# Kernel tuning notes

Hardware: AMD Instinct MI355X
Metric: run time of the kernel (lower is better)

Reference implementation:

```python
import jax, jax.numpy as jnp
import numpy as np

LS, LT, B = 48, 48, 64
VS, VT = 32000, 32000
E = 512      # src/tgt embed dim
HE = 512     # encoder hidden (BiLSTM -> context dim 2*HE)
HD = 512     # decoder hidden
PAD = 0


def setup_inputs() -> dict:
    key = jax.random.key(0)
    ks = iter(jax.random.split(key, 24))
    w = lambda *shape: jax.random.normal(next(ks), shape, dtype=jnp.float32) * 0.05
    inp = {}
    inp["xs"] = jax.random.randint(next(ks), (LS, B), 0, VS)
    inp["ts"] = jax.random.randint(next(ks), (LT, B), 0, VT)
    # embeddings (padding row zeroed, as nn.Embedding(padding_idx=0))
    inp["src_emb"] = w(VS, E).at[PAD].set(0.0)
    inp["tgt_emb"] = w(VT, E).at[PAD].set(0.0)
    # forward / backward encoder LSTMCells
    for p in ("encf", "encb"):
        inp[p + "_Wih"] = w(4 * HE, E)
        inp[p + "_Whh"] = w(4 * HE, HE)
        inp[p + "_bih"] = w(4 * HE)
        inp[p + "_bhh"] = w(4 * HE)
    # decoder LSTMCell: input = [tgt_emb ; o] -> E + HD
    inp["dec_Wih"] = w(4 * HD, E + HD)
    inp["dec_Whh"] = w(4 * HD, HD)
    inp["dec_bih"] = w(4 * HD)
    inp["dec_bhh"] = w(4 * HD)
    # MLPAttention: linear [2HE, HD+2HE] (no bias), v [1, 2HE] (no bias)
    inp["attn_W"] = w(2 * HE, HD + 2 * HE)
    inp["attn_v"] = w(1, 2 * HE)
    # decoder.linear: [HD, HD+2HE] with bias
    inp["lin_W"] = w(HD, HD + 2 * HE)
    inp["lin_b"] = w(HD)
    # decoder.linear_out: [VT, HD] with bias
    inp["out_W"] = w(VT, HD)
    inp["out_b"] = w(VT)
    return inp


def _lstm_cell(x, h, c, Wih, Whh, bih, bhh):
    g = x @ Wih.T + h @ Whh.T + (bih + bhh)
    i, f, gg, o = jnp.split(g, 4, axis=-1)  # torch gate order i,f,g,o
    c = jax.nn.sigmoid(f) * c + jax.nn.sigmoid(i) * jnp.tanh(gg)
    h = jax.nn.sigmoid(o) * jnp.tanh(c)
    return h, c


def _lstm_scan(embs, Wih, Whh, bih, bhh, hidden):
    bsz = embs.shape[1]
    init = (jnp.zeros((bsz, hidden), embs.dtype), jnp.zeros((bsz, hidden), embs.dtype))
    def step(carry, x):
        h, c = _lstm_cell(x, carry[0], carry[1], Wih, Whh, bih, bhh)
        return (h, c), h
    _, hs = jax.lax.scan(step, init, embs)
    return hs  # [L, B, hidden]


def reference(xs, ts, src_emb, tgt_emb,
              encf_Wih, encf_Whh, encf_bih, encf_bhh,
              encb_Wih, encb_Whh, encb_bih, encb_bhh,
              dec_Wih, dec_Whh, dec_bih, dec_bhh,
              attn_W, attn_v, lin_W, lin_b, out_W, out_b):
    # ---- BiLSTM encoder ----
    embs = src_emb[xs]                                   # [LS, B, E]
    hs_f = _lstm_scan(embs, encf_Wih, encf_Whh, encf_bih, encf_bhh, HE)
    hs_b = _lstm_scan(embs[::-1], encb_Wih, encb_Whh, encb_bih, encb_bhh, HE)[::-1]
    hs = jnp.concatenate([hs_f, hs_b], axis=2)           # [LS, B, 2HE]
    hs_bt = hs.transpose(1, 0, 2)                        # [B, LS, 2HE]

    # attention linear splits: cat((query, hs)) -> first HD cols act on query
    Wq, Wk = attn_W[:, :HD], attn_W[:, HD:]
    hs_proj = jnp.einsum('blk,hk->blh', hs_bt, Wk)       # precompute key part
    v = attn_v[0]

    ts_in, ts_out = ts[:-1], ts[1:]
    bsz = ts.shape[1]
    init = (jnp.zeros((bsz, HD), jnp.float32),) * 3      # h, m, o

    def dec_step(carry, t):
        h, m, o = carry
        emb = tgt_emb[t]                                 # [B, E]
        h, m = _lstm_cell(jnp.concatenate([emb, o], 1), h, m,
                          dec_Wih, dec_Whh, dec_bih, dec_bhh)
        # MLP attention
        score = jnp.tanh(hs_proj + (h @ Wq.T)[:, None, :]) @ v   # [B, LS]
        ps = jax.nn.softmax(score, axis=-1)
        c = jnp.einsum('bl,blh->bh', ps, hs_bt)          # [B, 2HE]
        o = jnp.tanh(jnp.concatenate([c, h], 1) @ lin_W.T + lin_b)
        logits = h @ out_W.T + out_b                     # [B, VT]
        return (h, m, o), logits

    _, logits = jax.lax.scan(dec_step, init, ts_in)      # [LT-1, B, VT]
    logp = jax.nn.log_softmax(logits, axis=-1)

    # NLLLoss(ignore_index=PAD), mean over non-pad targets
    nll = -jnp.take_along_axis(logp, ts_out[..., None], axis=-1)[..., 0]
    mask = (ts_out != PAD).astype(logp.dtype)
    return jnp.sum(nll * mask) / jnp.sum(mask)
```

## Files before the change

kernel.cpp:

```cpp
#include <hip/hip_runtime.h>
#include <stdint.h>

typedef unsigned short us;
typedef __attribute__((ext_vector_type(8))) short bf16x8;
typedef __attribute__((ext_vector_type(4))) float f32x4;

#define DI __device__ __forceinline__

constexpr int LS = 48, LT = 48, NB = 64, E = 512, H = 512, G = 2048, V = 32000;
constexpr int TD = LT - 1;
constexpr int MENC = LS * NB;
constexpr int MDEC = TD * NB;
constexpr int NCB = V / 64;

DI float bf2f(us u) { union { unsigned int i; float f; } c; c.i = ((unsigned int)u) << 16; return c.f; }
DI us f2bf(float f) { union { float f; unsigned int i; } c; c.f = f; return (us)((c.i + 0x7fffu + ((c.i >> 16) & 1u)) >> 16); }
DI float sigm(float x) { return 1.f / (1.f + __expf(-x)); }
DI float tanh_(float x) { x = fminf(15.f, fmaxf(-15.f, x)); float e = __expf(2.f * x); return (e - 1.f) / (e + 1.f); }

__global__ __launch_bounds__(256) void zero_k(float* p, int n) {
    int i = blockIdx.x * 256 + threadIdx.x;
    if (i < n) p[i] = 0.f;
}

__global__ __launch_bounds__(256) void conv_bf16(const float* __restrict__ src, int lds, int coff,
                                                 us* __restrict__ dst, int rows, int cols) {
    int i = blockIdx.x * 256 + threadIdx.x;
    if (i >= rows * cols) return;
    int r = i / cols, c = i % cols;
    dst[i] = f2bf(src[(size_t)r * lds + coff + c]);
}

__global__ __launch_bounds__(256) void gather_bf16(const int* __restrict__ idx, const float* __restrict__ emb,
                                                   us* __restrict__ dst) {
    int r = blockIdx.x;
    int id = idx[r];
    const float* s = emb + (size_t)id * E;
    us* d = dst + (size_t)r * E;
    for (int c = threadIdx.x; c < E; c += 256) d[c] = f2bf(s[c]);
}

__global__ __launch_bounds__(256) void pack_wcomb(const float* __restrict__ Wih, const float* __restrict__ Whh,
                                                  float* __restrict__ Wc) {
    int i = blockIdx.x * 256 + threadIdx.x;
    int j = i >> 10, c = i & 1023;
    Wc[i] = (c < 512) ? Wih[(size_t)j * 1024 + 512 + c] : Whh[(size_t)j * 512 + (c - 512)];
}

template <int EPI>
__global__ __launch_bounds__(256) void gemm16(const us* __restrict__ A, int lda,
                                              const us* __restrict__ W, int ldw,
                                              const float* __restrict__ b1, const float* __restrict__ b2,
                                              void* __restrict__ outp, int ldc, int K, int Mrows) {
    __shared__ us As[64][40];
    __shared__ us Ws[64][40];
    const int tid = threadIdx.x;
    const int m0 = blockIdx.y << 6, n0 = blockIdx.x << 6;
    const int srow = tid >> 2, sk = (tid & 3) << 3;
    const int l = tid & 63, w = tid >> 6;
    const int la = l & 15, lb = l >> 4;
    f32x4 acc[4] = {};
    const us* Aptr = A + (size_t)(m0 + srow) * lda + sk;
    const us* Wptr = W + (size_t)(n0 + srow) * ldw + sk;
    for (int k0 = 0; k0 < K; k0 += 32) {
        *(uint4*)&As[srow][sk] = *(const uint4*)(Aptr + k0);
        *(uint4*)&Ws[srow][sk] = *(const uint4*)(Wptr + k0);
        __syncthreads();
        bf16x8 af = *(bf16x8*)&As[(w << 4) + la][lb << 3];
#pragma unroll
        for (int c = 0; c < 4; c++) {
            bf16x8 bw = *(bf16x8*)&Ws[(c << 4) + la][lb << 3];
            acc[c] = __builtin_amdgcn_mfma_f32_16x16x32_bf16(af, bw, acc[c], 0, 0, 0);
        }
        __syncthreads();
    }
    if (EPI == 1) {
        us* O = (us*)outp;
#pragma unroll
        for (int c = 0; c < 4; c++) {
            int col = n0 + (c << 4) + la;
            float badd = (b1 ? b1[col] : 0.f) + (b2 ? b2[col] : 0.f);
#pragma unroll
            for (int r = 0; r < 4; r++) {
                int row = m0 + (w << 4) + (lb << 2) + r;
                O[(size_t)row * ldc + col] = f2bf(acc[c][r] + badd);
            }
        }
    } else {
        float* S = (float*)outp;
        float x[4][4];
#pragma unroll
        for (int c = 0; c < 4; c++) {
            int col = n0 + (c << 4) + la;
            float badd = b1[col];
#pragma unroll
            for (int r = 0; r < 4; r++) x[c][r] = acc[c][r] + badd;
        }
#pragma unroll
        for (int r = 0; r < 4; r++) {
            float lm = fmaxf(fmaxf(x[0][r], x[1][r]), fmaxf(x[2][r], x[3][r]));
#pragma unroll
            for (int mk = 1; mk < 16; mk <<= 1) lm = fmaxf(lm, __shfl_xor(lm, mk));
            float ls = __expf(x[0][r] - lm) + __expf(x[1][r] - lm) + __expf(x[2][r] - lm) + __expf(x[3][r] - lm);
#pragma unroll
            for (int mk = 1; mk < 16; mk <<= 1) ls += __shfl_xor(ls, mk);
            if (la == 0) {
                int row = m0 + (w << 4) + (lb << 2) + r;
                size_t o = ((size_t)blockIdx.x * Mrows + row) * 2;
                S[o] = lm;
                S[o + 1] = ls;
            }
        }
    }
}

__global__ __launch_bounds__(256) void enc_step(const us* __restrict__ gxf, const us* __restrict__ gxb,
                                                const float* __restrict__ Whhf, const float* __restrict__ Whhb,
                                                const float* __restrict__ hinf, const float* __restrict__ hinb,
                                                float* __restrict__ houtf, float* __restrict__ houtb,
                                                float* __restrict__ cf, float* __restrict__ cb_,
                                                float* __restrict__ hs, us* __restrict__ hs_bf, int s) {
    const int dir = blockIdx.z;
    const us* gx = dir ? gxb : gxf;
    const float* Whh = dir ? Whhb : Whhf;
    const float* hin = dir ? hinb : hinf;
    float* hout = dir ? houtb : houtf;
    float* cst = dir ? cb_ : cf;
    const int lrow = dir ? (LS - 1 - s) : s;
    __shared__ float hls[16][516];
    const int tid = threadIdx.x;
    const int bl = tid & 15, jl = tid >> 4;
    const int b0 = blockIdx.y * 16;
    const int j = blockIdx.x * 16 + jl;
    for (int idx = tid; idx < 16 * 512; idx += 256) { int r = idx >> 9, c = idx & 511; hls[r][c] = hin[(size_t)(b0 + r) * 512 + c]; }
    __syncthreads();
    const int b = b0 + bl;
    const us* grow = gx + ((size_t)lrow * NB + b) * G;
    float ai = bf2f(grow[j]), af = bf2f(grow[512 + j]), ag = bf2f(grow[1024 + j]), ao = bf2f(grow[1536 + j]);
    const float* wi = Whh + (size_t)j * 512;
    const float* wf = Whh + (size_t)(512 + j) * 512;
    const float* wg = Whh + (size_t)(1024 + j) * 512;
    const float* wo = Whh + (size_t)(1536 + j) * 512;
    for (int k = 0; k < 512; k += 4) {
        float4 h4 = *(float4*)&hls[bl][k];
        float4 a = *(const float4*)&wi[k]; ai += a.x * h4.x + a.y * h4.y + a.z * h4.z + a.w * h4.w;
        float4 f = *(const float4*)&wf[k]; af += f.x * h4.x + f.y * h4.y + f.z * h4.z + f.w * h4.w;
        float4 g = *(const float4*)&wg[k]; ag += g.x * h4.x + g.y * h4.y + g.z * h4.z + g.w * h4.w;
        float4 o = *(const float4*)&wo[k]; ao += o.x * h4.x + o.y * h4.y + o.z * h4.z + o.w * h4.w;
    }
    const int ci = b * 512 + j;
    float cn = sigm(af) * cst[ci] + sigm(ai) * tanh_(ag);
    float hn = sigm(ao) * tanh_(cn);
    cst[ci] = cn;
    hout[ci] = hn;
    size_t hso = ((size_t)lrow * NB + b) * 1024 + dir * 512 + j;
    hs[hso] = hn;
    hs_bf[hso] = f2bf(hn);
}

__global__ __launch_bounds__(256) void dec_cell(const us* __restrict__ gemb, const float* __restrict__ Wcomb,
                                                const float* __restrict__ oin, const float* __restrict__ hin,
                                                float* __restrict__ hout, float* __restrict__ cst,
                                                us* __restrict__ hdec_bf, int t) {
    __shared__ float uls[8][1028];
    const int tid = threadIdx.x;
    const int bl = tid & 7, jl = tid >> 3;
    const int b0 = blockIdx.y * 8;
    const int j = blockIdx.x * 32 + jl;
    for (int idx = tid; idx < 8 * 1024; idx += 256) {
        int r = idx >> 10, c = idx & 1023;
        uls[r][c] = (c < 512) ? oin[(size_t)(b0 + r) * 512 + c] : hin[(size_t)(b0 + r) * 512 + (c - 512)];
    }
    __syncthreads();
    const int b = b0 + bl;
    const us* grow = gemb + ((size_t)t * NB + b) * G;
    float ai = bf2f(grow[j]), af = bf2f(grow[512 + j]), ag = bf2f(grow[1024 + j]), ao = bf2f(grow[1536 + j]);
    const float* wi = Wcomb + (size_t)j * 1024;
    const float* wf = Wcomb + (size_t)(512 + j) * 1024;
    const float* wg = Wcomb + (size_t)(1024 + j) * 1024;
    const float* wo = Wcomb + (size_t)(1536 + j) * 1024;
    for (int k = 0; k < 1024; k += 4) {
        float4 h4 = *(float4*)&uls[bl][k];
        float4 a = *(const float4*)&wi[k]; ai += a.x * h4.x + a.y * h4.y + a.z * h4.z + a.w * h4.w;
        float4 f = *(const float4*)&wf[k]; af += f.x * h4.x + f.y * h4.y + f.z * h4.z + f.w * h4.w;
        float4 g = *(const float4*)&wg[k]; ag += g.x * h4.x + g.y * h4.y + g.z * h4.z + g.w * h4.w;
        float4 o = *(const float4*)&wo[k]; ao += o.x * h4.x + o.y * h4.y + o.z * h4.z + o.w * h4.w;
    }
    const int ci = b * 512 + j;
    float cn = sigm(af) * cst[ci] + sigm(ai) * tanh_(ag);
    float hn = sigm(ao) * tanh_(cn);
    cst[ci] = cn;
    hout[ci] = hn;
    hdec_bf[((size_t)t * NB + b) * 512 + j] = f2bf(hn);
}

template <int ACT>
__global__ __launch_bounds__(256) void small_gemm(const float* __restrict__ U1, int K1,
                                                  const float* __restrict__ U2, int K2,
                                                  const float* __restrict__ W, int ldw,
                                                  const float* __restrict__ bias,
                                                  float* __restrict__ out, int ldo) {
    extern __shared__ float uls[];
    const int K = K1 + K2;
    const int stride = K + 4;
    const int tid = threadIdx.x;
    for (int r = 0; r < 8; r++) {
        int gb = blockIdx.y * 8 + r;
        for (int c = tid; c < K; c += 256) {
            float v = (c < K1) ? U1[(size_t)gb * K1 + c] : U2[(size_t)gb * K2 + (c - K1)];
            uls[r * stride + c] = v;
        }
    }
    __syncthreads();
    const int bl = tid & 7, jl = tid >> 3;
    const int b = blockIdx.y * 8 + bl;
    const int n = blockIdx.x * 32 + jl;
    const float* wr = W + (size_t)n * ldw;
    float acc = 0.f;
    for (int k = 0; k < K; k += 4) {
        float4 u = *(float4*)&uls[bl * stride + k];
        float4 wv = *(const float4*)&wr[k];
        acc += u.x * wv.x + u.y * wv.y + u.z * wv.z + u.w * wv.w;
    }
    if (bias) acc += bias[n];
    if (ACT == 1) acc = tanh_(acc);
    out[(size_t)b * ldo + n] = acc;
}

__global__ __launch_bounds__(256) void dec_attn(const float* __restrict__ qbuf, const us* __restrict__ hsproj,
                                                const float* __restrict__ hs, const float* __restrict__ vat,
                                                float* __restrict__ catt) {
    const int b = blockIdx.x;
    const int tid = threadIdx.x;
    const int w = tid >> 6, l = tid & 63;
    __shared__ float sc[48];
    __shared__ float ps[48];
    float qv[16], vv[16];
#pragma unroll
    for (int i = 0; i < 16; i++) { qv[i] = qbuf[(size_t)b * 1024 + l * 16 + i]; vv[i] = vat[l * 16 + i]; }
    for (int li = w * 12; li < w * 12 + 12; ++li) {
        const us* hp = hsproj + ((size_t)li * NB + b) * 1024 + l * 16;
        float p = 0.f;
#pragma unroll
        for (int i = 0; i < 16; i++) p += vv[i] * tanh_(bf2f(hp[i]) + qv[i]);
#pragma unroll
        for (int m = 1; m < 64; m <<= 1) p += __shfl_xor(p, m);
        if (l == 0) sc[li] = p;
    }
    __syncthreads();
    if (w == 0) {
        float x = (l < 48) ? sc[l] : -1e30f;
        float mx = x;
#pragma unroll
        for (int m = 1; m < 64; m <<= 1) mx = fmaxf(mx, __shfl_xor(mx, m));
        float e = (l < 48) ? __expf(x - mx) : 0.f;
        float s = e;
#pragma unroll
        for (int m = 1; m < 64; m <<= 1) s += __shfl_xor(s, m);
        if (l < 48) ps[l] = e / s;
    }
    __syncthreads();
    float a0 = 0, a1 = 0, a2 = 0, a3 = 0;
    for (int li = 0; li < 48; ++li) {
        float p = ps[li];
        float4 hv = *(const float4*)(hs + ((size_t)li * NB + b) * 1024 + tid * 4);
        a0 += p * hv.x; a1 += p * hv.y; a2 += p * hv.z; a3 += p * hv.w;
    }
    float4 r; r.x = a0; r.y = a1; r.z = a2; r.w = a3;
    *(float4*)(catt + (size_t)b * 1024 + tid * 4) = r;
}

__global__ __launch_bounds__(256) void tgt_kernel(const us* __restrict__ hdec_bf, const us* __restrict__ woutbf,
                                                  const float* __restrict__ out_b, const int* __restrict__ ts,
                                                  float* __restrict__ tgt) {
    int wid = blockIdx.x * 4 + (threadIdx.x >> 6);
    int l = threadIdx.x & 63;
    int t = wid >> 6, b = wid & 63;
    int tg = ts[(t + 1) * NB + b];
    const us* hr = hdec_bf + (size_t)wid * 512 + l * 8;
    const us* wr = woutbf + (size_t)tg * 512 + l * 8;
    float acc = 0.f;
#pragma unroll
    for (int i = 0; i < 8; i++) acc += bf2f(hr[i]) * bf2f(wr[i]);
#pragma unroll
    for (int m = 1; m < 64; m <<= 1) acc += __shfl_xor(acc, m);
    if (l == 0) tgt[wid] = acc + out_b[tg];
}

__global__ __launch_bounds__(256) void stats_reduce(const float* __restrict__ stats, const float* __restrict__ tgt,
                                                    const int* __restrict__ ts, float* __restrict__ sums) {
    int r = blockIdx.x * 256 + threadIdx.x;
    float nll = 0.f, mk = 0.f;
    if (r < MDEC) {
        float M = -1e30f, S = 0.f;
        for (int cb = 0; cb < NCB; ++cb) {
            float m = stats[((size_t)cb * MDEC + r) * 2];
            float s = stats[((size_t)cb * MDEC + r) * 2 + 1];
            if (m > M) { S = S * __expf(M - m) + s; M = m; }
            else { S += s * __expf(m - M); }
        }
        float logZ = M + __logf(S);
        int t = r >> 6, b = r & 63;
        int tg = ts[(t + 1) * NB + b];
        mk = (tg != 0) ? 1.f : 0.f;
        nll = (logZ - tgt[r]) * mk;
    }
#pragma unroll
    for (int m = 1; m < 64; m <<= 1) { nll += __shfl_xor(nll, m); mk += __shfl_xor(mk, m); }
    if ((threadIdx.x & 63) == 0) { atomicAdd(&sums[0], nll); atomicAdd(&sums[1], mk); }
}

__global__ void final_div(const float* __restrict__ sums, float* __restrict__ out) { out[0] = sums[0] / sums[1]; }

extern "C" void kernel_launch(void* const* d_in, const int* in_sizes, int n_in,
                              void* d_out, int out_size, void* d_ws, size_t ws_size,
                              hipStream_t stream) {
    const int* xs = (const int*)d_in[0];
    const int* ts = (const int*)d_in[1];
    const float* src_emb = (const float*)d_in[2];
    const float* tgt_emb = (const float*)d_in[3];
    const float* encf_Wih = (const float*)d_in[4];
    const float* encf_Whh = (const float*)d_in[5];
    const float* encf_bih = (const float*)d_in[6];
    const float* encf_bhh = (const float*)d_in[7];
    const float* encb_Wih = (const float*)d_in[8];
    const float* encb_Whh = (const float*)d_in[9];
    const float* encb_bih = (const float*)d_in[10];
    const float* encb_bhh = (const float*)d_in[11];
    const float* dec_Wih = (const float*)d_in[12];
    const float* dec_Whh = (const float*)d_in[13];
    const float* dec_bih = (const float*)d_in[14];
    const float* dec_bhh = (const float*)d_in[15];
    const float* attn_W = (const float*)d_in[16];
    const float* attn_v = (const float*)d_in[17];
    const float* lin_W = (const float*)d_in[18];
    const float* lin_b = (const float*)d_in[19];
    const float* out_W = (const float*)d_in[20];
    const float* out_b = (const float*)d_in[21];

    char* p = (char*)d_ws;
    auto alloc = [&](size_t bytes) { void* r = (void*)p; p += (bytes + 255) & ~(size_t)255; return r; };

    float* hf0 = (float*)alloc(NB * 512 * 4);
    float* hb0 = (float*)alloc(NB * 512 * 4);
    float* cf = (float*)alloc(NB * 512 * 4);
    float* cb = (float*)alloc(NB * 512 * 4);
    float* hd0 = (float*)alloc(NB * 512 * 4);
    float* cd = (float*)alloc(NB * 512 * 4);
    float* od = (float*)alloc(NB * 512 * 4);
    float* sums = (float*)alloc(2 * 4);
    const int ZN = 7 * NB * 512 + 64;

    float* hf1 = (float*)alloc(NB * 512 * 4);
    float* hb1 = (float*)alloc(NB * 512 * 4);
    float* hd1 = (float*)alloc(NB * 512 * 4);
    float* wcomb = (float*)alloc((size_t)G * 1024 * 4);
    float* hs = (float*)alloc((size_t)MENC * 1024 * 4);
    float* qbuf = (float*)alloc((size_t)NB * 1024 * 4);
    float* catt = (float*)alloc((size_t)NB * 1024 * 4);
    float* stats = (float*)alloc((size_t)NCB * MDEC * 2 * 4);
    float* tgtl = (float*)alloc((size_t)MDEC * 4);

    us* embs_bf = (us*)alloc((size_t)MENC * E * 2);
    us* tembs_bf = (us*)alloc((size_t)MDEC * E * 2);
    us* wfih_bf = (us*)alloc((size_t)G * 512 * 2);
    us* wbih_bf = (us*)alloc((size_t)G * 512 * 2);
    us* wdE_bf = (us*)alloc((size_t)G * 512 * 2);
    us* wk_bf = (us*)alloc((size_t)1024 * 1024 * 2);
    us* wout_bf = (us*)alloc((size_t)V * 512 * 2);
    us* gxf_bf = (us*)alloc((size_t)MENC * G * 2);
    us* gxb_bf = (us*)alloc((size_t)MENC * G * 2);
    us* gemb_bf = (us*)alloc((size_t)MDEC * G * 2);
    us* hs_bf = (us*)alloc((size_t)MENC * 1024 * 2);
    us* hsproj_bf = (us*)alloc((size_t)MENC * 1024 * 2);
    us* hdec_bf = (us*)alloc((size_t)MDEC * 512 * 2);

    zero_k<<<dim3((ZN + 255) / 256), 256, 0, stream>>>(hf0, ZN);

    conv_bf16<<<dim3((G * 512 + 255) / 256), 256, 0, stream>>>(encf_Wih, 512, 0, wfih_bf, G, 512);
    conv_bf16<<<dim3((G * 512 + 255) / 256), 256, 0, stream>>>(encb_Wih, 512, 0, wbih_bf, G, 512);
    conv_bf16<<<dim3((G * 512 + 255) / 256), 256, 0, stream>>>(dec_Wih, 1024, 0, wdE_bf, G, 512);
    conv_bf16<<<dim3((1024 * 1024 + 255) / 256), 256, 0, stream>>>(attn_W, 1536, 512, wk_bf, 1024, 1024);
    conv_bf16<<<dim3((V * 512 + 255) / 256), 256, 0, stream>>>(out_W, 512, 0, wout_bf, V, 512);
    pack_wcomb<<<dim3(G * 1024 / 256), 256, 0, stream>>>(dec_Wih, dec_Whh, wcomb);

    gather_bf16<<<dim3(MENC), 256, 0, stream>>>(xs, src_emb, embs_bf);
    gather_bf16<<<dim3(MDEC), 256, 0, stream>>>(ts, tgt_emb, tembs_bf);

    gemm16<1><<<dim3(G / 64, MENC / 64), 256, 0, stream>>>(embs_bf, 512, wfih_bf, 512, encf_bih, encf_bhh, gxf_bf, G, 512, 0);
    gemm16<1><<<dim3(G / 64, MENC / 64), 256, 0, stream>>>(embs_bf, 512, wbih_bf, 512, encb_bih, encb_bhh, gxb_bf, G, 512, 0);
    gemm16<1><<<dim3(G / 64, MDEC / 64), 256, 0, stream>>>(tembs_bf, 512, wdE_bf, 512, dec_bih, dec_bhh, gemb_bf, G, 512, 0);

    for (int s = 0; s < LS; ++s) {
        const float* hinf = (s & 1) ? hf1 : hf0; float* houtf = (s & 1) ? hf0 : hf1;
        const float* hinb = (s & 1) ? hb1 : hb0; float* houtb = (s & 1) ? hb0 : hb1;
        enc_step<<<dim3(32, 4, 2), 256, 0, stream>>>(gxf_bf, gxb_bf, encf_Whh, encb_Whh,
                                                     hinf, hinb, houtf, houtb, cf, cb, hs, hs_bf, s);
    }

    gemm16<1><<<dim3(1024 / 64, MENC / 64), 256, 0, stream>>>(hs_bf, 1024, wk_bf, 1024, nullptr, nullptr, hsproj_bf, 1024, 1024, 0);

    for (int t = 0; t < TD; ++t) {
        const float* hin = (t & 1) ? hd1 : hd0; float* hout = (t & 1) ? hd0 : hd1;
        dec_cell<<<dim3(16, 8), 256, 0, stream>>>(gemb_bf, wcomb, od, hin, hout, cd, hdec_bf, t);
        if (t < TD - 1) {
            small_gemm<0><<<dim3(32, 8), 256, (512 + 4) * 8 * 4, stream>>>(hout, 512, nullptr, 0, attn_W, 1536, nullptr, qbuf, 1024);
            dec_attn<<<dim3(NB), 256, 0, stream>>>(qbuf, hsproj_bf, hs, attn_v, catt);
            small_gemm<1><<<dim3(16, 8), 256, (1536 + 4) * 8 * 4, stream>>>(catt, 1024, hout, 512, lin_W, 1536, lin_b, od, 512);
        }
    }

    gemm16<2><<<dim3(NCB, MDEC / 64), 256, 0, stream>>>(hdec_bf, 512, wout_bf, 512, out_b, nullptr, stats, 0, 512, MDEC);

    tgt_kernel<<<dim3(MDEC / 4), 256, 0, stream>>>(hdec_bf, wout_bf, out_b, ts, tgtl);
    stats_reduce<<<dim3((MDEC + 255) / 256), 256, 0, stream>>>(stats, tgtl, ts, sums);
    final_div<<<dim3(1), 1, 0, stream>>>(sums, (float*)d_out);
}
```

Before: 7.473 ms.

## Replace per-step encoder/decoder launches with persistent cooperative kernels using grid sync

The encoder loop of 48 launches and the decoder loop of roughly 188 launches become two persistent cooperative kernels. Each kernel keeps its cell state in registers and uses grid-wide syncs between steps and phases. The decoder kernel fuses the LSTM cell, query projection, attention and output linear, splits K across lane pairs, and reads lin_W and the context from bf16 copies, which drops the fp32 hs buffer. This removes launch overhead and intermediate round-trips, at the cost of grid-sync latency and some bf16 precision loss in the attention context and linear layer.

```diff
diff --git a/kernel.cpp b/kernel.cpp
--- a/kernel.cpp
+++ b/kernel.cpp
@@ -1,5 +1,8 @@
 #include <hip/hip_runtime.h>
+#include <hip/hip_cooperative_groups.h>
 #include <stdint.h>
+
+namespace cg = cooperative_groups;
 
 typedef unsigned short us;
 typedef __attribute__((ext_vector_type(8))) short bf16x8;
@@ -7,7 +10,7 @@
 
 #define DI __device__ __forceinline__
 
-constexpr int LS = 48, LT = 48, NB = 64, E = 512, H = 512, G = 2048, V = 32000;
+constexpr int LS = 48, LT = 48, NB = 64, E = 512, G = 2048, V = 32000;
 constexpr int TD = LT - 1;
 constexpr int MENC = LS * NB;
 constexpr int MDEC = TD * NB;
@@ -114,160 +117,191 @@
     }
 }
 
-__global__ __launch_bounds__(256) void enc_step(const us* __restrict__ gxf, const us* __restrict__ gxb,
+__global__ __launch_bounds__(256) void enc_coop(const us* __restrict__ gxf, const us* __restrict__ gxb,
                                                 const float* __restrict__ Whhf, const float* __restrict__ Whhb,
-                                                const float* __restrict__ hinf, const float* __restrict__ hinb,
-                                                float* __restrict__ houtf, float* __restrict__ houtb,
-                                                float* __restrict__ cf, float* __restrict__ cb_,
-                                                float* __restrict__ hs, us* __restrict__ hs_bf, int s) {
-    const int dir = blockIdx.z;
+                                                float* __restrict__ hA, float* __restrict__ hB,
+                                                us* __restrict__ hs_bf) {
+    cg::grid_group gg = cg::this_grid();
+    const int bx = blockIdx.x;
+    const int jt = bx & 31, btile = (bx >> 5) & 3, dir = bx >> 7;
     const us* gx = dir ? gxb : gxf;
     const float* Whh = dir ? Whhb : Whhf;
-    const float* hin = dir ? hinb : hinf;
-    float* hout = dir ? houtb : houtf;
-    float* cst = dir ? cb_ : cf;
-    const int lrow = dir ? (LS - 1 - s) : s;
+    const int tid = threadIdx.x, bl = tid & 15, jl = tid >> 4;
+    const int b0 = btile * 16, b = b0 + bl, j = jt * 16 + jl;
     __shared__ float hls[16][516];
-    const int tid = threadIdx.x;
-    const int bl = tid & 15, jl = tid >> 4;
-    const int b0 = blockIdx.y * 16;
-    const int j = blockIdx.x * 16 + jl;
-    for (int idx = tid; idx < 16 * 512; idx += 256) { int r = idx >> 9, c = idx & 511; hls[r][c] = hin[(size_t)(b0 + r) * 512 + c]; }
-    __syncthreads();
-    const int b = b0 + bl;
-    const us* grow = gx + ((size_t)lrow * NB + b) * G;
-    float ai = bf2f(grow[j]), af = bf2f(grow[512 + j]), ag = bf2f(grow[1024 + j]), ao = bf2f(grow[1536 + j]);
+    float cstate = 0.f;
     const float* wi = Whh + (size_t)j * 512;
     const float* wf = Whh + (size_t)(512 + j) * 512;
     const float* wg = Whh + (size_t)(1024 + j) * 512;
     const float* wo = Whh + (size_t)(1536 + j) * 512;
-    for (int k = 0; k < 512; k += 4) {
-        float4 h4 = *(float4*)&hls[bl][k];
-        float4 a = *(const float4*)&wi[k]; ai += a.x * h4.x + a.y * h4.y + a.z * h4.z + a.w * h4.w;
-        float4 f = *(const float4*)&wf[k]; af += f.x * h4.x + f.y * h4.y + f.z * h4.z + f.w * h4.w;
-        float4 g = *(const float4*)&wg[k]; ag += g.x * h4.x + g.y * h4.y + g.z * h4.z + g.w * h4.w;
-        float4 o = *(const float4*)&wo[k]; ao += o.x * h4.x + o.y * h4.y + o.z * h4.z + o.w * h4.w;
-    }
-    const int ci = b * 512 + j;
-    float cn = sigm(af) * cst[ci] + sigm(ai) * tanh_(ag);
-    float hn = sigm(ao) * tanh_(cn);
-    cst[ci] = cn;
-    hout[ci] = hn;
-    size_t hso = ((size_t)lrow * NB + b) * 1024 + dir * 512 + j;
-    hs[hso] = hn;
-    hs_bf[hso] = f2bf(hn);
-}
-
-__global__ __launch_bounds__(256) void dec_cell(const us* __restrict__ gemb, const float* __restrict__ Wcomb,
-                                                const float* __restrict__ oin, const float* __restrict__ hin,
-                                                float* __restrict__ hout, float* __restrict__ cst,
-                                                us* __restrict__ hdec_bf, int t) {
-    __shared__ float uls[8][1028];
+    const size_t dof = (size_t)dir * NB * 512;
+    for (int s = 0; s < LS; ++s) {
+        const float* hin = ((s & 1) ? hB : hA) + dof;
+        float* hout = ((s & 1) ? hA : hB) + dof;
+        const int lrow = dir ? (LS - 1 - s) : s;
+        for (int idx = tid; idx < 16 * 512; idx += 256) {
+            int r = idx >> 9, c = idx & 511;
+            hls[r][c] = hin[(size_t)(b0 + r) * 512 + c];
+        }
+        __syncthreads();
+        const us* grow = gx + ((size_t)lrow * NB + b) * G;
+        float ai = bf2f(grow[j]), af = bf2f(grow[512 + j]), ag = bf2f(grow[1024 + j]), ao = bf2f(grow[1536 + j]);
+        for (int k = 0; k < 512; k += 4) {
+            float4 h4 = *(float4*)&hls[bl][k];
+            float4 a = *(const float4*)&wi[k]; ai += a.x * h4.x + a.y * h4.y + a.z * h4.z + a.w * h4.w;
+            float4 f = *(const float4*)&wf[k]; af += f.x * h4.x + f.y * h4.y + f.z * h4.z + f.w * h4.w;
+            float4 g = *(const float4*)&wg[k]; ag += g.x * h4.x + g.y * h4.y + g.z * h4.z + g.w * h4.w;
+            float4 o = *(const float4*)&wo[k]; ao += o.x * h4.x + o.y * h4.y + o.z * h4.z + o.w * h4.w;
+        }
+        float cn = sigm(af) * cstate + sigm(ai) * tanh_(ag);
+        float hn = sigm(ao) * tanh_(cn);
+        cstate = cn;
+        hout[(size_t)b * 512 + j] = hn;
+        hs_bf[((size_t)lrow * NB + b) * 1024 + dir * 512 + j] = f2bf(hn);
+        gg.sync();
+    }
+}
+
+__global__ __launch_bounds__(256) void dec_coop(const us* __restrict__ gemb, const float* __restrict__ Wcomb,
+                                                const float* __restrict__ attn_W, const float* __restrict__ attn_v,
+                                                const us* __restrict__ hsproj, const us* __restrict__ hs_bf,
+                                                const us* __restrict__ linw_bf, const float* __restrict__ lin_b,
+                                                float* __restrict__ h0, float* __restrict__ h1,
+                                                float* __restrict__ od, float* __restrict__ qbuf,
+                                                us* __restrict__ hdec_bf) {
+    cg::grid_group gg = cg::this_grid();
     const int tid = threadIdx.x;
-    const int bl = tid & 7, jl = tid >> 3;
-    const int b0 = blockIdx.y * 8;
-    const int j = blockIdx.x * 32 + jl;
-    for (int idx = tid; idx < 8 * 1024; idx += 256) {
-        int r = idx >> 10, c = idx & 1023;
-        uls[r][c] = (c < 512) ? oin[(size_t)(b0 + r) * 512 + c] : hin[(size_t)(b0 + r) * 512 + (c - 512)];
-    }
-    __syncthreads();
-    const int b = b0 + bl;
-    const us* grow = gemb + ((size_t)t * NB + b) * G;
-    float ai = bf2f(grow[j]), af = bf2f(grow[512 + j]), ag = bf2f(grow[1024 + j]), ao = bf2f(grow[1536 + j]);
-    const float* wi = Wcomb + (size_t)j * 1024;
-    const float* wf = Wcomb + (size_t)(512 + j) * 1024;
-    const float* wg = Wcomb + (size_t)(1024 + j) * 1024;
-    const float* wo = Wcomb + (size_t)(1536 + j) * 1024;
-    for (int k = 0; k < 1024; k += 4) {
-        float4 h4 = *(float4*)&uls[bl][k];
-        float4 a = *(const float4*)&wi[k]; ai += a.x * h4.x + a.y * h4.y + a.z * h4.z + a.w * h4.w;
-        float4 f = *(const float4*)&wf[k]; af += f.x * h4.x + f.y * h4.y + f.z * h4.z + f.w * h4.w;
-        float4 g = *(const float4*)&wg[k]; ag += g.x * h4.x + g.y * h4.y + g.z * h4.z + g.w * h4.w;
-        float4 o = *(const float4*)&wo[k]; ao += o.x * h4.x + o.y * h4.y + o.z * h4.z + o.w * h4.w;
-    }
-    const int ci = b * 512 + j;
-    float cn = sigm(af) * cst[ci] + sigm(ai) * tanh_(ag);
-    float hn = sigm(ao) * tanh_(cn);
-    cst[ci] = cn;
-    hout[ci] = hn;
-    hdec_bf[((size_t)t * NB + b) * 512 + j] = f2bf(hn);
-}
-
-template <int ACT>
-__global__ __launch_bounds__(256) void small_gemm(const float* __restrict__ U1, int K1,
-                                                  const float* __restrict__ U2, int K2,
-                                                  const float* __restrict__ W, int ldw,
-                                                  const float* __restrict__ bias,
-                                                  float* __restrict__ out, int ldo) {
-    extern __shared__ float uls[];
-    const int K = K1 + K2;
-    const int stride = K + 4;
-    const int tid = threadIdx.x;
-    for (int r = 0; r < 8; r++) {
-        int gb = blockIdx.y * 8 + r;
-        for (int c = tid; c < K; c += 256) {
-            float v = (c < K1) ? U1[(size_t)gb * K1 + c] : U2[(size_t)gb * K2 + (c - K1)];
-            uls[r * stride + c] = v;
-        }
-    }
-    __syncthreads();
-    const int bl = tid & 7, jl = tid >> 3;
-    const int b = blockIdx.y * 8 + bl;
-    const int n = blockIdx.x * 32 + jl;
-    const float* wr = W + (size_t)n * ldw;
-    float acc = 0.f;
-    for (int k = 0; k < K; k += 4) {
-        float4 u = *(float4*)&uls[bl * stride + k];
-        float4 wv = *(const float4*)&wr[k];
-        acc += u.x * wv.x + u.y * wv.y + u.z * wv.z + u.w * wv.w;
-    }
-    if (bias) acc += bias[n];
-    if (ACT == 1) acc = tanh_(acc);
-    out[(size_t)b * ldo + n] = acc;
-}
-
-__global__ __launch_bounds__(256) void dec_attn(const float* __restrict__ qbuf, const us* __restrict__ hsproj,
-                                                const float* __restrict__ hs, const float* __restrict__ vat,
-                                                float* __restrict__ catt) {
-    const int b = blockIdx.x;
-    const int tid = threadIdx.x;
-    const int w = tid >> 6, l = tid & 63;
-    __shared__ float sc[48];
-    __shared__ float ps[48];
-    float qv[16], vv[16];
-#pragma unroll
-    for (int i = 0; i < 16; i++) { qv[i] = qbuf[(size_t)b * 1024 + l * 16 + i]; vv[i] = vat[l * 16 + i]; }
-    for (int li = w * 12; li < w * 12 + 12; ++li) {
-        const us* hp = hsproj + ((size_t)li * NB + b) * 1024 + l * 16;
-        float p = 0.f;
-#pragma unroll
-        for (int i = 0; i < 16; i++) p += vv[i] * tanh_(bf2f(hp[i]) + qv[i]);
-#pragma unroll
-        for (int m = 1; m < 64; m <<= 1) p += __shfl_xor(p, m);
-        if (l == 0) sc[li] = p;
-    }
-    __syncthreads();
-    if (w == 0) {
-        float x = (l < 48) ? sc[l] : -1e30f;
-        float mx = x;
-#pragma unroll
-        for (int m = 1; m < 64; m <<= 1) mx = fmaxf(mx, __shfl_xor(mx, m));
-        float e = (l < 48) ? __expf(x - mx) : 0.f;
-        float s = e;
-#pragma unroll
-        for (int m = 1; m < 64; m <<= 1) s += __shfl_xor(s, m);
-        if (l < 48) ps[l] = e / s;
-    }
-    __syncthreads();
-    float a0 = 0, a1 = 0, a2 = 0, a3 = 0;
-    for (int li = 0; li < 48; ++li) {
-        float p = ps[li];
-        float4 hv = *(const float4*)(hs + ((size_t)li * NB + b) * 1024 + tid * 4);
-        a0 += p * hv.x; a1 += p * hv.y; a2 += p * hv.z; a3 += p * hv.w;
-    }
-    float4 r; r.x = a0; r.y = a1; r.z = a2; r.w = a3;
-    *(float4*)(catt + (size_t)b * 1024 + tid * 4) = r;
+    const int bx = blockIdx.x;
+    __shared__ float uls[8][1044];
+    __shared__ float u2ls[1544];
+    __shared__ float sls[48], pls[48];
+
+    const int khA = tid & 1, blA = (tid >> 1) & 7, jlA = tid >> 4;
+    const int bgrp = bx >> 5, jt = bx & 31;
+    const int bA = bgrp * 8 + blA, jA = jt * 16 + jlA;
+    const int blB = tid & 7, nlB = tid >> 3;
+    const int bB = bgrp * 8 + blB, nB = jt * 32 + nlB;
+    const int bC = bx >> 2, qtr = bx & 3;
+    const int wC = tid >> 6, lC = tid & 63;
+
+    float cstate = 0.f;
+    const float* wiA = Wcomb + ((size_t)jA) * 1024 + khA * 512;
+    const float* wfA = Wcomb + ((size_t)(512 + jA)) * 1024 + khA * 512;
+    const float* wgA = Wcomb + ((size_t)(1024 + jA)) * 1024 + khA * 512;
+    const float* woA = Wcomb + ((size_t)(1536 + jA)) * 1024 + khA * 512;
+
+    float vv[16];
+#pragma unroll
+    for (int i = 0; i < 16; i++) vv[i] = attn_v[lC * 16 + i];
+
+    for (int t = 0; t < TD; ++t) {
+        const float* hprev = (t & 1) ? h1 : h0;
+        float* hnext = (t & 1) ? h0 : h1;
+        {
+            const int b0 = bgrp * 8;
+            for (int idx = tid; idx < 8 * 1024; idx += 256) {
+                int r = idx >> 10, c = idx & 1023;
+                uls[r][c] = (c < 512) ? od[(size_t)(b0 + r) * 512 + c]
+                                      : hprev[(size_t)(b0 + r) * 512 + (c - 512)];
+            }
+            __syncthreads();
+            float ai = 0.f, af = 0.f, ag = 0.f, ao = 0.f;
+            const float* u = &uls[blA][khA * 512];
+            for (int k = 0; k < 512; k += 4) {
+                float4 h4 = *(float4*)&u[k];
+                float4 a = *(const float4*)&wiA[k]; ai += a.x * h4.x + a.y * h4.y + a.z * h4.z + a.w * h4.w;
+                float4 f = *(const float4*)&wfA[k]; af += f.x * h4.x + f.y * h4.y + f.z * h4.z + f.w * h4.w;
+                float4 g = *(const float4*)&wgA[k]; ag += g.x * h4.x + g.y * h4.y + g.z * h4.z + g.w * h4.w;
+                float4 o = *(const float4*)&woA[k]; ao += o.x * h4.x + o.y * h4.y + o.z * h4.z + o.w * h4.w;
+            }
+            ai += __shfl_xor(ai, 1); af += __shfl_xor(af, 1);
+            ag += __shfl_xor(ag, 1); ao += __shfl_xor(ao, 1);
+            if (khA == 0) {
+                const us* grow = gemb + ((size_t)t * NB + bA) * G;
+                ai += bf2f(grow[jA]); af += bf2f(grow[512 + jA]);
+                ag += bf2f(grow[1024 + jA]); ao += bf2f(grow[1536 + jA]);
+                float cn = sigm(af) * cstate + sigm(ai) * tanh_(ag);
+                float hn = sigm(ao) * tanh_(cn);
+                cstate = cn;
+                hnext[(size_t)bA * 512 + jA] = hn;
+                hdec_bf[((size_t)t * NB + bA) * 512 + jA] = f2bf(hn);
+            }
+        }
+        gg.sync();
+        if (t < TD - 1) {
+            for (int idx = tid; idx < 8 * 512; idx += 256) {
+                int r = idx >> 9, c = idx & 511;
+                uls[r][c] = hnext[(size_t)(bgrp * 8 + r) * 512 + c];
+            }
+            __syncthreads();
+            const float* wq = attn_W + (size_t)nB * 1536;
+            const float* u = &uls[blB][0];
+            float acc = 0.f;
+            for (int k = 0; k < 512; k += 4) {
+                float4 h4 = *(float4*)&u[k];
+                float4 wv = *(const float4*)&wq[k];
+                acc += h4.x * wv.x + h4.y * wv.y + h4.z * wv.z + h4.w * wv.w;
+            }
+            qbuf[(size_t)bB * 1024 + nB] = acc;
+        }
+        gg.sync();
+        if (t < TD - 1) {
+            float qv[16];
+#pragma unroll
+            for (int i = 0; i < 16; i++) qv[i] = qbuf[(size_t)bC * 1024 + lC * 16 + i];
+            for (int c = tid; c < 512; c += 256) u2ls[1024 + c] = hnext[(size_t)bC * 512 + c];
+            for (int li = wC * 12; li < wC * 12 + 12; ++li) {
+                const us* hp = hsproj + ((size_t)li * NB + bC) * 1024 + lC * 16;
+                float p = 0.f;
+#pragma unroll
+                for (int i = 0; i < 16; i++) p += vv[i] * tanh_(bf2f(hp[i]) + qv[i]);
+#pragma unroll
+                for (int m = 1; m < 64; m <<= 1) p += __shfl_xor(p, m);
+                if (lC == 0) sls[li] = p;
+            }
+            __syncthreads();
+            if (wC == 0) {
+                float x = (lC < 48) ? sls[lC] : -1e30f;
+                float mx = x;
+#pragma unroll
+                for (int m = 1; m < 64; m <<= 1) mx = fmaxf(mx, __shfl_xor(mx, m));
+                float e = (lC < 48) ? __expf(x - mx) : 0.f;
+                float s = e;
+#pragma unroll
+                for (int m = 1; m < 64; m <<= 1) s += __shfl_xor(s, m);
+                if (lC < 48) pls[lC] = e / s;
+            }
+            __syncthreads();
+            {
+                int d0 = tid * 4;
+                float a0 = 0, a1 = 0, a2 = 0, a3 = 0;
+                for (int li = 0; li < 48; ++li) {
+                    float pw = pls[li];
+                    const us* hv = hs_bf + ((size_t)li * NB + bC) * 1024 + d0;
+                    a0 += pw * bf2f(hv[0]); a1 += pw * bf2f(hv[1]);
+                    a2 += pw * bf2f(hv[2]); a3 += pw * bf2f(hv[3]);
+                }
+                u2ls[d0] = a0; u2ls[d0 + 1] = a1; u2ls[d0 + 2] = a2; u2ls[d0 + 3] = a3;
+            }
+            __syncthreads();
+            {
+                int d = qtr * 128 + (tid >> 1);
+                int kh2 = tid & 1;
+                const us* wr = linw_bf + (size_t)d * 1536 + kh2 * 768;
+                const float* u2 = &u2ls[kh2 * 768];
+                float acc = 0.f;
+                for (int k = 0; k < 768; k += 8) {
+                    float4 ua = *(const float4*)&u2[k];
+                    float4 ub = *(const float4*)&u2[k + 4];
+                    acc += bf2f(wr[k]) * ua.x + bf2f(wr[k + 1]) * ua.y + bf2f(wr[k + 2]) * ua.z + bf2f(wr[k + 3]) * ua.w;
+                    acc += bf2f(wr[k + 4]) * ub.x + bf2f(wr[k + 5]) * ub.y + bf2f(wr[k + 6]) * ub.z + bf2f(wr[k + 7]) * ub.w;
+                }
+                acc += __shfl_xor(acc, 1);
+                if (kh2 == 0) od[(size_t)bC * 512 + d] = tanh_(acc + lin_b[d]);
+            }
+        }
+        gg.sync();
+    }
 }
 
 __global__ __launch_bounds__(256) void tgt_kernel(const us* __restrict__ hdec_bf, const us* __restrict__ woutbf,
@@ -343,21 +377,16 @@
 
     float* hf0 = (float*)alloc(NB * 512 * 4);
     float* hb0 = (float*)alloc(NB * 512 * 4);
-    float* cf = (float*)alloc(NB * 512 * 4);
-    float* cb = (float*)alloc(NB * 512 * 4);
     float* hd0 = (float*)alloc(NB * 512 * 4);
-    float* cd = (float*)alloc(NB * 512 * 4);
     float* od = (float*)alloc(NB * 512 * 4);
     float* sums = (float*)alloc(2 * 4);
-    const int ZN = 7 * NB * 512 + 64;
+    const int ZN = 4 * NB * 512 + 64;
 
     float* hf1 = (float*)alloc(NB * 512 * 4);
     float* hb1 = (float*)alloc(NB * 512 * 4);
     float* hd1 = (float*)alloc(NB * 512 * 4);
     float* wcomb = (float*)alloc((size_t)G * 1024 * 4);
-    float* hs = (float*)alloc((size_t)MENC * 1024 * 4);
     float* qbuf = (float*)alloc((size_t)NB * 1024 * 4);
-    float* catt = (float*)alloc((size_t)NB * 1024 * 4);
     float* stats = (float*)alloc((size_t)NCB * MDEC * 2 * 4);
     float* tgtl = (float*)alloc((size_t)MDEC * 4);
 
@@ -367,6 +396,7 @@
     us* wbih_bf = (us*)alloc((size_t)G * 512 * 2);
     us* wdE_bf = (us*)alloc((size_t)G * 512 * 2);
     us* wk_bf = (us*)alloc((size_t)1024 * 1024 * 2);
+    us* linw_bf = (us*)alloc((size_t)512 * 1536 * 2);
     us* wout_bf = (us*)alloc((size_t)V * 512 * 2);
     us* gxf_bf = (us*)alloc((size_t)MENC * G * 2);
     us* gxb_bf = (us*)alloc((size_t)MENC * G * 2);
@@ -381,6 +411,7 @@
     conv_bf16<<<dim3((G * 512 + 255) / 256), 256, 0, stream>>>(encb_Wih, 512, 0, wbih_bf, G, 512);
     conv_bf16<<<dim3((G * 512 + 255) / 256), 256, 0, stream>>>(dec_Wih, 1024, 0, wdE_bf, G, 512);
     conv_bf16<<<dim3((1024 * 1024 + 255) / 256), 256, 0, stream>>>(attn_W, 1536, 512, wk_bf, 1024, 1024);
+    conv_bf16<<<dim3((512 * 1536 + 255) / 256), 256, 0, stream>>>(lin_W, 1536, 0, linw_bf, 512, 1536);
     conv_bf16<<<dim3((V * 512 + 255) / 256), 256, 0, stream>>>(out_W, 512, 0, wout_bf, V, 512);
     pack_wcomb<<<dim3(G * 1024 / 256), 256, 0, stream>>>(dec_Wih, dec_Whh, wcomb);
 
@@ -391,23 +422,27 @@
     gemm16<1><<<dim3(G / 64, MENC / 64), 256, 0, stream>>>(embs_bf, 512, wbih_bf, 512, encb_bih, encb_bhh, gxb_bf, G, 512, 0);
     gemm16<1><<<dim3(G / 64, MDEC / 64), 256, 0, stream>>>(tembs_bf, 512, wdE_bf, 512, dec_bih, dec_bhh, gemb_bf, G, 512, 0);
 
-    for (int s = 0; s < LS; ++s) {
-        const float* hinf = (s & 1) ? hf1 : hf0; float* houtf = (s & 1) ? hf0 : hf1;
-        const float* hinb = (s & 1) ? hb1 : hb0; float* houtb = (s & 1) ? hb0 : hb1;
-        enc_step<<<dim3(32, 4, 2), 256, 0, stream>>>(gxf_bf, gxb_bf, encf_Whh, encb_Whh,
-                                                     hinf, hinb, houtf, houtb, cf, cb, hs, hs_bf, s);
+    {
+        const us* a0 = gxf_bf; const us* a1 = gxb_bf;
+        const float* a2 = encf_Whh; const float* a3 = encb_Whh;
+        float* a4 = hf0; float* a5 = hf1;
+        us* a6 = hs_bf;
+        void* args[] = { &a0, &a1, &a2, &a3, &a4, &a5, &a6 };
+        hipLaunchCooperativeKernel((void*)enc_coop, dim3(256), dim3(256), args, 0, stream);
     }
 
     gemm16<1><<<dim3(1024 / 64, MENC / 64), 256, 0, stream>>>(hs_bf, 1024, wk_bf, 1024, nullptr, nullptr, hsproj_bf, 1024, 1024, 0);
 
-    for (int t = 0; t < TD; ++t) {
-        const float* hin = (t & 1) ? hd1 : hd0; float* hout = (t & 1) ? hd0 : hd1;
-        dec_cell<<<dim3(16, 8), 256, 0, stream>>>(gemb_bf, wcomb, od, hin, hout, cd, hdec_bf, t);
-        if (t < TD - 1) {
-            small_gemm<0><<<dim3(32, 8), 256, (512 + 4) * 8 * 4, stream>>>(hout, 512, nullptr, 0, attn_W, 1536, nullptr, qbuf, 1024);
-            dec_attn<<<dim3(NB), 256, 0, stream>>>(qbuf, hsproj_bf, hs, attn_v, catt);
-            small_gemm<1><<<dim3(16, 8), 256, (1536 + 4) * 8 * 4, stream>>>(catt, 1024, hout, 512, lin_W, 1536, lin_b, od, 512);
-        }
+    {
+        const us* a0 = gemb_bf; const float* a1 = wcomb;
+        const float* a2 = attn_W; const float* a3 = attn_v;
+        const us* a4 = hsproj_bf; const us* a5 = hs_bf;
+        const us* a6 = linw_bf; const float* a7 = lin_b;
+        float* a8 = hd0; float* a9 = hd1;
+        float* a10 = od; float* a11 = qbuf;
+        us* a12 = hdec_bf;
+        void* args[] = { &a0, &a1, &a2, &a3, &a4, &a5, &a6, &a7, &a8, &a9, &a10, &a11, &a12 };
+        hipLaunchCooperativeKernel((void*)dec_coop, dim3(256), dim3(256), args, 0, stream);
     }
 
     gemm16<2><<<dim3(NCB, MDEC / 64), 256, 0, stream>>>(hdec_bf, 512, wout_bf, 512, out_b, nullptr, stats, 0, 512, MDEC);
```

New measurement: 10.29 ms. +37.8%, slower.
